# Optimization experiments

Hardware: AMD Instinct MI355X
Metric: run time of the kernel (lower is better)

The kernel has to match this reference:

```python
import jax, jax.numpy as jnp
import numpy as np

EPS = 1e-5  # torch InstanceNorm2d default eps


def instance_norm(x):
    # normalize over spatial dims (H, W) per sample, per channel; affine=False
    mean = jnp.mean(x, axis=(2, 3), keepdims=True)
    var = jnp.var(x, axis=(2, 3), keepdims=True)  # biased var, matching torch
    return (x - mean) * jax.lax.rsqrt(var + EPS)


def conv1x1(x, w, b):
    # x: [B,C,H,W], w: [O,C], b: [O] -> [B,O,H,W]
    return jnp.einsum('oc,bchw->bohw', w, x) + b[None, :, None, None]


def setup_inputs() -> dict:
    key = jax.random.key(0)
    ks = jax.random.split(key, 9)
    B, C, H, W = 4, 64, 96, 96
    fan_out = C  # 1x1 conv: fan_out = out_ch * 1 * 1
    std = float(np.sqrt(2.0 / fan_out))  # kaiming_normal_, mode='fan_out', relu
    x = jax.random.normal(ks[0], (B, C, H, W), dtype=jnp.float32)
    wq = jax.random.normal(ks[1], (C, C), dtype=jnp.float32) * std
    wk = jax.random.normal(ks[2], (C, C), dtype=jnp.float32) * std
    wv = jax.random.normal(ks[3], (C, C), dtype=jnp.float32) * std
    wo = jax.random.normal(ks[4], (C, C), dtype=jnp.float32) * std
    bq = jnp.zeros((C,), dtype=jnp.float32)
    bk = jnp.zeros((C,), dtype=jnp.float32)
    bv = jnp.zeros((C,), dtype=jnp.float32)
    bo = jnp.zeros((C,), dtype=jnp.float32)
    return {"x": x, "wq": wq, "bq": bq, "wk": wk, "bk": bk,
            "wv": wv, "bv": bv, "wo": wo, "bo": bo}


def reference(x, wq, bq, wk, bk, wv, bv, wo, bo):
    B, C, H, W = x.shape
    h = instance_norm(x)
    q = conv1x1(h, wq, bq)  # [B,C,H,W]
    k = conv1x1(h, wk, bk)
    v = conv1x1(h, wv, bv)
    N = H * W
    q = q.reshape(B, C, N).transpose(0, 2, 1)  # [B,N,C]
    k = k.reshape(B, C, N)                     # [B,C,N]
    v = v.reshape(B, C, N).transpose(0, 2, 1)  # [B,N,C]
    scores = jnp.einsum('bnc,bcm->bnm', q, k) * (C ** -0.5)  # [B,N,N]
    attn = jax.nn.softmax(scores, axis=-1)
    o = jnp.einsum('bnm,bmc->bnc', attn, v)  # [B,N,C]
    o = o.reshape(B, H, W, C).transpose(0, 3, 1, 2)  # [B,C,H,W]
    o = conv1x1(o, wo, bo)
    return x + o
```

## Files before the change

### kernel.cpp

```cpp
#include <hip/hip_runtime.h>
#include <stdint.h>

#define BB 4
#define CCH 64
#define NN 9216
#define NTILES 144
#define FTILES 72
#define NCHUNK 3
#define CHUNKK 3072

typedef unsigned short u16;
typedef __attribute__((ext_vector_type(8))) short bhalf8;
typedef __attribute__((ext_vector_type(4))) float f32x4;
typedef __attribute__((ext_vector_type(4))) u16 u16x4;
typedef __attribute__((ext_vector_type(8))) u16 u16x8;
typedef __attribute__((ext_vector_type(2))) unsigned int u32x2;

#define MFMA16(a, b, c) __builtin_amdgcn_mfma_f32_16x16x32_bf16((a), (b), (c), 0, 0, 0)

static __device__ __forceinline__ u16 f2bf(float f) {
  union { float f; unsigned u; } v; v.f = f;
  return (u16)((v.u + 0x7fffu + ((v.u >> 16) & 1u)) >> 16);
}
static __device__ __forceinline__ float bf2f(u16 h) {
  union { unsigned u; float f; } v; v.u = ((unsigned)h) << 16; return v.f;
}
static __device__ __forceinline__ unsigned pk2(float lo, float hi) {
  unsigned a = __float_as_uint(hi) + 0x8000u;
  unsigned b = __float_as_uint(lo) + 0x8000u;
  return __builtin_amdgcn_perm(a, b, 0x07060302u);
}
static __device__ __forceinline__ void glds16(const void* g, void* l) {
  __builtin_amdgcn_global_load_lds(
      (const __attribute__((address_space(1))) unsigned int*)g,
      (__attribute__((address_space(3))) unsigned int*)l, 16, 0, 0);
}

extern "C" __global__ __launch_bounds__(256) void prep_kernel(
    const float* __restrict__ x,
    const float* __restrict__ wq, const float* __restrict__ wk,
    const float* __restrict__ wv, const float* __restrict__ wo,
    float* __restrict__ mean, float* __restrict__ rstd, u16* __restrict__ wbf) {
  if (blockIdx.x >= 256) {
    int i = (blockIdx.x - 256) * 256 + threadIdx.x;
    const float* src = (i < 4096) ? wq : (i < 8192) ? wk : (i < 12288) ? wv : wo;
    wbf[i] = f2bf(src[i & 4095]);
    return;
  }
  int idx = blockIdx.x;
  const float* p = x + (size_t)idx * NN;
  float s = 0.f, ss = 0.f;
  for (int i = threadIdx.x; i < NN; i += 256) { float v = p[i]; s += v; ss += v * v; }
#pragma unroll
  for (int o = 32; o > 0; o >>= 1) { s += __shfl_xor(s, o, 64); ss += __shfl_xor(ss, o, 64); }
  __shared__ float ls[4], lss[4];
  int w = threadIdx.x >> 6;
  if ((threadIdx.x & 63) == 0) { ls[w] = s; lss[w] = ss; }
  __syncthreads();
  if (threadIdx.x == 0) {
    s = ls[0] + ls[1] + ls[2] + ls[3];
    ss = lss[0] + lss[1] + lss[2] + lss[3];
    float m = s * (1.f / NN);
    float var = ss * (1.f / NN) - m * m;
    mean[idx] = m;
    rstd[idx] = rsqrtf(var + 1e-5f);
  }
}

extern "C" __global__ __launch_bounds__(256, 4) void qkv_kernel(
    const float* __restrict__ x,
    const float* __restrict__ mean, const float* __restrict__ rstd,
    const u16* __restrict__ wqb, const u16* __restrict__ wkb, const u16* __restrict__ wvb,
    const float* __restrict__ bq, const float* __restrict__ bk,
    u16* __restrict__ Qt, u16* __restrict__ Kt, u16* __restrict__ Vt) {
  __shared__ u16 hbuf[64 * 72];
  int b = blockIdx.x / NTILES, tile = blockIdx.x % NTILES;
  int n0 = tile * 64;
  int t = threadIdx.x;
  int w = t >> 6, lane = t & 63, q = lane >> 4, ln = lane & 15;
  const float QSCALE = 0.125f * 1.44269504088896340736f;
#pragma unroll
  for (int rep = 0; rep < 16; rep++) {
    int c = rep * 4 + w;
    float v = x[(size_t)(b * 64 + c) * NN + n0 + lane];
    float h = (v - mean[b * 64 + c]) * rstd[b * 64 + c];
    hbuf[lane * 72 + c] = f2bf(h);
  }
  __syncthreads();
  int hrow = (16 * w + ln) * 72;
  bhalf8 hb0 = *(const bhalf8*)&hbuf[hrow + q * 8];
  bhalf8 hb1 = *(const bhalf8*)&hbuf[hrow + 32 + q * 8];
  size_t nrow = (size_t)(b * NN + n0 + 16 * w + ln) * 64;
#pragma unroll
  for (int ct = 0; ct < 4; ct++) {
    int wrow = (16 * ct + ln) * 64;
    bhalf8 a0 = *(const bhalf8*)&wqb[wrow + q * 8];
    bhalf8 a1 = *(const bhalf8*)&wqb[wrow + 32 + q * 8];
    f32x4 d = {0.f, 0.f, 0.f, 0.f};
    d = MFMA16(a0, hb0, d);
    d = MFMA16(a1, hb1, d);
    f32x4 b4 = *(const f32x4*)&bq[16 * ct + 4 * q];
    u16x4 pk;
#pragma unroll
    for (int r = 0; r < 4; r++) pk[r] = f2bf((d[r] + b4[r]) * QSCALE);
    *(u16x4*)&Qt[nrow + 16 * ct + 4 * q] = pk;
  }
#pragma unroll
  for (int ct = 0; ct < 4; ct++) {
    int wrow = (16 * ct + ln) * 64;
    bhalf8 a0 = *(const bhalf8*)&wkb[wrow + q * 8];
    bhalf8 a1 = *(const bhalf8*)&wkb[wrow + 32 + q * 8];
    f32x4 d = {0.f, 0.f, 0.f, 0.f};
    d = MFMA16(a0, hb0, d);
    d = MFMA16(a1, hb1, d);
    f32x4 b4 = *(const f32x4*)&bk[16 * ct + 4 * q];
    u16x4 pk;
#pragma unroll
    for (int r = 0; r < 4; r++) pk[r] = f2bf(d[r] + b4[r]);
    *(u16x4*)&Kt[nrow + 16 * ct + 4 * q] = pk;
  }
#pragma unroll
  for (int ct = 0; ct < 4; ct++) {
    int wrow = (16 * ct + ln) * 64;
    bhalf8 b0 = *(const bhalf8*)&wvb[wrow + q * 8];
    bhalf8 b1 = *(const bhalf8*)&wvb[wrow + 32 + q * 8];
    f32x4 d = {0.f, 0.f, 0.f, 0.f};
    d = MFMA16(hb0, b0, d);
    d = MFMA16(hb1, b1, d);
    u16x4 pk;
#pragma unroll
    for (int r = 0; r < 4; r++) pk[r] = f2bf(d[r]);
    *(u16x4*)&Vt[(size_t)(b * 64 + 16 * ct + ln) * NN + n0 + 16 * w + 4 * q] = pk;
  }
}

extern "C" __global__ __launch_bounds__(256, 4) void flash_kernel(
    const u16* __restrict__ Qt, const u16* __restrict__ Kt, const u16* __restrict__ Vt,
    u16* __restrict__ Opart, float* __restrict__ Lsum) {
  __shared__ u16 kbuf[64 * 64];
  __shared__ u16 vbuf[64 * 64];
  __shared__ u16 pbuf[4 * 32 * 64];
  int blk = blockIdx.x;
  int b = blk / (FTILES * NCHUNK);
  int rem = blk % (FTILES * NCHUNK);
  int tile = rem / NCHUNK, chunk = rem % NCHUNK;
  int m_start = chunk * CHUNKK;
  int t = threadIdx.x;
  int w = t >> 6, lane = t & 63, q = lane >> 4, ln = lane & 15;
  int n0w = tile * 128 + 32 * w;
  const u16* qp = Qt + (size_t)(b * NN + n0w + ln) * 64 + q * 8;
  bhalf8 qa0 = *(const bhalf8*)qp;
  bhalf8 qa1 = *(const bhalf8*)(qp + 32);
  bhalf8 qb0 = *(const bhalf8*)(qp + 16 * 64);
  bhalf8 qb1 = *(const bhalf8*)(qp + 16 * 64 + 32);
  const short ONE = 0x3F80;
  const bhalf8 ones = {ONE, ONE, ONE, ONE, ONE, ONE, ONE, ONE};
  f32x4 oa[4], ob[4];
  f32x4 lacc_a = {0.f, 0.f, 0.f, 0.f}, lacc_b = {0.f, 0.f, 0.f, 0.f};
#pragma unroll
  for (int i = 0; i < 4; i++) { oa[i] = (f32x4){0.f,0.f,0.f,0.f}; ob[i] = (f32x4){0.f,0.f,0.f,0.f}; }
  u16* pb = pbuf + w * 2048;
  int row_s = 16 * w + (lane >> 3);
  int usw = (lane & 7) ^ (row_s & 7);
  const u16* kgp = Kt + ((size_t)b * NN + m_start + row_s) * 64 + usw * 8;
  const u16* vgp = Vt + (size_t)(b * 64 + row_s) * NN + m_start + usw * 8;
  u16* klds = &kbuf[w * 1024];
  u16* vlds = &vbuf[w * 1024];
  int sbase = (q ^ (ln & 7)) * 8;

  for (int m0 = 0; m0 < CHUNKK; m0 += 64) {
    __syncthreads();
    glds16(kgp, klds);
    glds16(kgp + 512, klds + 512);
    glds16(vgp, vlds);
    glds16(vgp + (size_t)8 * NN, vlds + 512);
    kgp += 64 * 64;
    vgp += 64;
    __syncthreads();

    f32x4 sa[4], sb[4];
#pragma unroll
    for (int mt = 0; mt < 4; mt++) {
      int krow = (16 * mt + ln) * 64;
      bhalf8 ka0 = *(const bhalf8*)&kbuf[krow + sbase];
      bhalf8 ka1 = *(const bhalf8*)&kbuf[krow + (sbase ^ 32)];
      f32x4 acc = {0.f, 0.f, 0.f, 0.f};
      acc = MFMA16(ka0, qa0, acc);
      acc = MFMA16(ka1, qa1, acc);
      sa[mt] = acc;
      f32x4 acc2 = {0.f, 0.f, 0.f, 0.f};
      acc2 = MFMA16(ka0, qb0, acc2);
      acc2 = MFMA16(ka1, qb1, acc2);
      sb[mt] = acc2;
    }
#pragma unroll
    for (int mt = 0; mt < 4; mt++) {
      f32x4 pa, pbv;
#pragma unroll
      for (int r = 0; r < 4; r++) {
        pa[r] = __builtin_amdgcn_exp2f(sa[mt][r]);
        pbv[r] = __builtin_amdgcn_exp2f(sb[mt][r]);
      }
      int pu = (((2 * mt + (q >> 1)) ^ (ln & 7)) << 3) + ((q & 1) << 2);
      u32x2 pk;
      pk[0] = pk2(pa[0], pa[1]);
      pk[1] = pk2(pa[2], pa[3]);
      *(u32x2*)&pb[ln * 64 + pu] = pk;
      pk[0] = pk2(pbv[0], pbv[1]);
      pk[1] = pk2(pbv[2], pbv[3]);
      *(u32x2*)&pb[(16 + ln) * 64 + pu] = pk;
    }
#pragma unroll
    for (int s2 = 0; s2 < 2; s2++) {
      bhalf8 pfa = *(const bhalf8*)&pb[ln * 64 + (sbase ^ (32 * s2))];
      bhalf8 pfb = *(const bhalf8*)&pb[(16 + ln) * 64 + (sbase ^ (32 * s2))];
      lacc_a = MFMA16(ones, pfa, lacc_a);
      lacc_b = MFMA16(ones, pfb, lacc_b);
#pragma unroll
      for (int ct = 0; ct < 4; ct++) {
        int vrow = (16 * ct + ln) * 64;
        bhalf8 va = *(const bhalf8*)&vbuf[vrow + (sbase ^ (32 * s2))];
        oa[ct] = MFMA16(va, pfa, oa[ct]);
        ob[ct] = MFMA16(va, pfb, ob[ct]);
      }
    }
  }
  size_t pbase = (size_t)blk * (128 * 64);
  int ra = 32 * w + ln, rb = ra + 16;
#pragma unroll
  for (int ct = 0; ct < 4; ct++) {
    u32x2 pka, pkb;
    pka[0] = pk2(oa[ct][0], oa[ct][1]); pka[1] = pk2(oa[ct][2], oa[ct][3]);
    pkb[0] = pk2(ob[ct][0], ob[ct][1]); pkb[1] = pk2(ob[ct][2], ob[ct][3]);
    *(u32x2*)&Opart[pbase + (size_t)ra * 64 + 16 * ct + 4 * q] = pka;
    *(u32x2*)&Opart[pbase + (size_t)rb * 64 + 16 * ct + 4 * q] = pkb;
  }
  if (q == 0) {
    float* lb_ = Lsum + (size_t)blk * 128;
    lb_[ra] = lacc_a[0];
    lb_[rb] = lacc_b[0];
  }
}

extern "C" __global__ __launch_bounds__(256, 4) void out_kernel(
    const float* __restrict__ x, const u16* __restrict__ wob, const float* __restrict__ bo,
    const u16* __restrict__ Opart, const float* __restrict__ Lsum, const float* __restrict__ bv,
    float* __restrict__ out) {
  int b = blockIdx.x / NTILES, tile = blockIdx.x % NTILES;
  int t = threadIdx.x;
  int w = t >> 6, lane = t & 63, q = lane >> 4, ln = lane & 15;
  int n0w = tile * 64 + 16 * w;
  int ptile = tile >> 1;
  int prow = (tile & 1) * 64 + 16 * w + ln;
  int p0 = (b * FTILES + ptile) * NCHUNK;
  float L = 0.f;
  float acc0[8], acc1[8];
#pragma unroll
  for (int j = 0; j < 8; j++) { acc0[j] = 0.f; acc1[j] = 0.f; }
#pragma unroll
  for (int ch = 0; ch < NCHUNK; ch++) {
    L += Lsum[(size_t)(p0 + ch) * 128 + prow];
    const u16* op = Opart + ((size_t)(p0 + ch) * 128 + prow) * 64;
    u16x8 d0 = *(const u16x8*)(op + 8 * q);
    u16x8 d1 = *(const u16x8*)(op + 32 + 8 * q);
#pragma unroll
    for (int j = 0; j < 8; j++) { acc0[j] += bf2f(d0[j]); acc1[j] += bf2f(d1[j]); }
  }
  float rl = 1.0f / L;
  union { u16x8 us; bhalf8 bh; } A0, A1;
#pragma unroll
  for (int j = 0; j < 8; j++) {
    A0.us[j] = f2bf(acc0[j] * rl + bv[8 * q + j]);
    A1.us[j] = f2bf(acc1[j] * rl + bv[32 + 8 * q + j]);
  }
  bhalf8 a0 = A0.bh, a1 = A1.bh;
#pragma unroll
  for (int ct = 0; ct < 4; ct++) {
    int wrow = (16 * ct + ln) * 64;
    bhalf8 b0 = *(const bhalf8*)&wob[wrow + q * 8];
    bhalf8 b1 = *(const bhalf8*)&wob[wrow + 32 + q * 8];
    f32x4 d = {0.f, 0.f, 0.f, 0.f};
    d = MFMA16(a0, b0, d);
    d = MFMA16(a1, b1, d);
    int co = 16 * ct + ln;
    size_t base = (size_t)(b * 64 + co) * NN + n0w + 4 * q;
    f32x4 xv = *(const f32x4*)&x[base];
    float bc = bo[co];
    f32x4 ov;
#pragma unroll
    for (int r = 0; r < 4; r++) ov[r] = xv[r] + bc + d[r];
    *(f32x4*)&out[base] = ov;
  }
}

extern "C" void kernel_launch(void* const* d_in, const int* in_sizes, int n_in,
                              void* d_out, int out_size, void* d_ws, size_t ws_size,
                              hipStream_t stream) {
  (void)in_sizes; (void)n_in; (void)out_size; (void)ws_size;
  const float* x  = (const float*)d_in[0];
  const float* wq = (const float*)d_in[1];
  const float* bq = (const float*)d_in[2];
  const float* wk = (const float*)d_in[3];
  const float* bk = (const float*)d_in[4];
  const float* wv = (const float*)d_in[5];
  const float* bv = (const float*)d_in[6];
  const float* wo = (const float*)d_in[7];
  const float* bo = (const float*)d_in[8];
  float* out = (float*)d_out;
  char* ws = (char*)d_ws;
  float* mean = (float*)ws;
  float* rstd = (float*)(ws + 1024);
  u16* wbf = (u16*)(ws + 2048);
  u16* Qt = (u16*)(ws + 36864);
  u16* Kt = Qt + (size_t)BB * NN * 64;
  u16* Vt = Kt + (size_t)BB * NN * 64;
  u16* Opart = Vt + (size_t)BB * NN * 64;
  float* Lsum = (float*)(Opart + (size_t)BB * FTILES * NCHUNK * 128 * 64);
  const u16* wqb = wbf;
  const u16* wkb = wbf + 4096;
  const u16* wvb = wbf + 8192;
  const u16* wob = wbf + 12288;

  prep_kernel<<<320, 256, 0, stream>>>(x, wq, wk, wv, wo, mean, rstd, wbf);
  qkv_kernel<<<BB * NTILES, 256, 0, stream>>>(x, mean, rstd, wqb, wkb, wvb, bq, bk, Qt, Kt, Vt);
  flash_kernel<<<BB * FTILES * NCHUNK, 256, 0, stream>>>(Qt, Kt, Vt, Opart, Lsum);
  out_kernel<<<BB * NTILES, 256, 0, stream>>>(x, wob, bo, Opart, Lsum, bv, out);
}
```

Baseline: 220.7 us.

## Double-buffer K/V LDS tiles in flash kernel and split score/P stages into halves

The flash kernel now double-buffers the K and V shared-memory tiles, prefetching the next 64-key tile while computing on the current one. This drops one of the two barriers per iteration and hides global-to-LDS latency. The score, exp and P·V work is split into two 32-key halves with a smaller per-wave P buffer, which lowers register and LDS pressure. The qkv kernel's normalize/transpose stage also changes so each thread handles four consecutive channels and writes them to LDS as one packed store. The cost is twice the K/V LDS footprint, which may affect occupancy.

```diff
diff --git a/kernel.cpp b/kernel.cpp
--- a/kernel.cpp
+++ b/kernel.cpp
@@ -79,12 +79,20 @@
   int t = threadIdx.x;
   int w = t >> 6, lane = t & 63, q = lane >> 4, ln = lane & 15;
   const float QSCALE = 0.125f * 1.44269504088896340736f;
-#pragma unroll
-  for (int rep = 0; rep < 16; rep++) {
-    int c = rep * 4 + w;
-    float v = x[(size_t)(b * 64 + c) * NN + n0 + lane];
-    float h = (v - mean[b * 64 + c]) * rstd[b * 64 + c];
-    hbuf[lane * 72 + c] = f2bf(h);
+  const float* mb = mean + b * 64;
+  const float* rb_ = rstd + b * 64;
+  int nloc = lane;
+#pragma unroll
+  for (int rep = 0; rep < 4; rep++) {
+    int c0 = 16 * w + 4 * rep;
+    float h0 = (x[(size_t)(b * 64 + c0 + 0) * NN + n0 + nloc] - mb[c0 + 0]) * rb_[c0 + 0];
+    float h1 = (x[(size_t)(b * 64 + c0 + 1) * NN + n0 + nloc] - mb[c0 + 1]) * rb_[c0 + 1];
+    float h2 = (x[(size_t)(b * 64 + c0 + 2) * NN + n0 + nloc] - mb[c0 + 2]) * rb_[c0 + 2];
+    float h3 = (x[(size_t)(b * 64 + c0 + 3) * NN + n0 + nloc] - mb[c0 + 3]) * rb_[c0 + 3];
+    u32x2 hp;
+    hp[0] = pk2(h0, h1);
+    hp[1] = pk2(h2, h3);
+    *(u32x2*)&hbuf[nloc * 72 + c0] = hp;
   }
   __syncthreads();
   int hrow = (16 * w + ln) * 72;
@@ -137,9 +145,9 @@
 extern "C" __global__ __launch_bounds__(256, 4) void flash_kernel(
     const u16* __restrict__ Qt, const u16* __restrict__ Kt, const u16* __restrict__ Vt,
     u16* __restrict__ Opart, float* __restrict__ Lsum) {
-  __shared__ u16 kbuf[64 * 64];
-  __shared__ u16 vbuf[64 * 64];
-  __shared__ u16 pbuf[4 * 32 * 64];
+  __shared__ u16 kbuf[2][64 * 64];
+  __shared__ u16 vbuf[2][64 * 64];
+  __shared__ u16 pbuf[4][16 * 64];
   int blk = blockIdx.x;
   int b = blk / (FTILES * NCHUNK);
   int rem = blk % (FTILES * NCHUNK);
@@ -159,67 +167,76 @@
   f32x4 lacc_a = {0.f, 0.f, 0.f, 0.f}, lacc_b = {0.f, 0.f, 0.f, 0.f};
 #pragma unroll
   for (int i = 0; i < 4; i++) { oa[i] = (f32x4){0.f,0.f,0.f,0.f}; ob[i] = (f32x4){0.f,0.f,0.f,0.f}; }
-  u16* pb = pbuf + w * 2048;
+  u16* pw = pbuf[w];
   int row_s = 16 * w + (lane >> 3);
   int usw = (lane & 7) ^ (row_s & 7);
   const u16* kgp = Kt + ((size_t)b * NN + m_start + row_s) * 64 + usw * 8;
   const u16* vgp = Vt + (size_t)(b * 64 + row_s) * NN + m_start + usw * 8;
-  u16* klds = &kbuf[w * 1024];
-  u16* vlds = &vbuf[w * 1024];
   int sbase = (q ^ (ln & 7)) * 8;
-
-  for (int m0 = 0; m0 < CHUNKK; m0 += 64) {
+  const int NIT = CHUNKK / 64;
+
+  {
+    u16* kl = &kbuf[0][w * 1024];
+    u16* vl = &vbuf[0][w * 1024];
+    glds16(kgp, kl); glds16(kgp + 512, kl + 512);
+    glds16(vgp, vl); glds16(vgp + (size_t)8 * NN, vl + 512);
+    kgp += 4096; vgp += 64;
+  }
+
+#pragma unroll 2
+  for (int i = 0; i < NIT; i++) {
     __syncthreads();
-    glds16(kgp, klds);
-    glds16(kgp + 512, klds + 512);
-    glds16(vgp, vlds);
-    glds16(vgp + (size_t)8 * NN, vlds + 512);
-    kgp += 64 * 64;
-    vgp += 64;
-    __syncthreads();
-
-    f32x4 sa[4], sb[4];
-#pragma unroll
-    for (int mt = 0; mt < 4; mt++) {
-      int krow = (16 * mt + ln) * 64;
-      bhalf8 ka0 = *(const bhalf8*)&kbuf[krow + sbase];
-      bhalf8 ka1 = *(const bhalf8*)&kbuf[krow + (sbase ^ 32)];
-      f32x4 acc = {0.f, 0.f, 0.f, 0.f};
-      acc = MFMA16(ka0, qa0, acc);
-      acc = MFMA16(ka1, qa1, acc);
-      sa[mt] = acc;
-      f32x4 acc2 = {0.f, 0.f, 0.f, 0.f};
-      acc2 = MFMA16(ka0, qb0, acc2);
-      acc2 = MFMA16(ka1, qb1, acc2);
-      sb[mt] = acc2;
+    if (i + 1 < NIT) {
+      u16* kl = &kbuf[(i + 1) & 1][w * 1024];
+      u16* vl = &vbuf[(i + 1) & 1][w * 1024];
+      glds16(kgp, kl); glds16(kgp + 512, kl + 512);
+      glds16(vgp, vl); glds16(vgp + (size_t)8 * NN, vl + 512);
+      kgp += 4096; vgp += 64;
     }
-#pragma unroll
-    for (int mt = 0; mt < 4; mt++) {
-      f32x4 pa, pbv;
-#pragma unroll
-      for (int r = 0; r < 4; r++) {
-        pa[r] = __builtin_amdgcn_exp2f(sa[mt][r]);
-        pbv[r] = __builtin_amdgcn_exp2f(sb[mt][r]);
+    const u16* kb = kbuf[i & 1];
+    const u16* vb = vbuf[i & 1];
+#pragma unroll
+    for (int p = 0; p < 2; p++) {
+      f32x4 s[4];
+#pragma unroll
+      for (int lm = 0; lm < 2; lm++) {
+        int mt = 2 * p + lm;
+        int krow = (16 * mt + ln) * 64;
+        bhalf8 ka0 = *(const bhalf8*)&kb[krow + sbase];
+        bhalf8 ka1 = *(const bhalf8*)&kb[krow + (sbase ^ 32)];
+        f32x4 acc = {0.f, 0.f, 0.f, 0.f};
+        acc = MFMA16(ka0, qa0, acc);
+        acc = MFMA16(ka1, qa1, acc);
+        s[2 * lm] = acc;
+        f32x4 acc2 = {0.f, 0.f, 0.f, 0.f};
+        acc2 = MFMA16(ka0, qb0, acc2);
+        acc2 = MFMA16(ka1, qb1, acc2);
+        s[2 * lm + 1] = acc2;
       }
-      int pu = (((2 * mt + (q >> 1)) ^ (ln & 7)) << 3) + ((q & 1) << 2);
-      u32x2 pk;
-      pk[0] = pk2(pa[0], pa[1]);
-      pk[1] = pk2(pa[2], pa[3]);
-      *(u32x2*)&pb[ln * 64 + pu] = pk;
-      pk[0] = pk2(pbv[0], pbv[1]);
-      pk[1] = pk2(pbv[2], pbv[3]);
-      *(u32x2*)&pb[(16 + ln) * 64 + pu] = pk;
-    }
-#pragma unroll
-    for (int s2 = 0; s2 < 2; s2++) {
-      bhalf8 pfa = *(const bhalf8*)&pb[ln * 64 + (sbase ^ (32 * s2))];
-      bhalf8 pfb = *(const bhalf8*)&pb[(16 + ln) * 64 + (sbase ^ (32 * s2))];
+#pragma unroll
+      for (int lm = 0; lm < 2; lm++) {
+        f32x4 pa, pbv;
+#pragma unroll
+        for (int r = 0; r < 4; r++) {
+          pa[r] = __builtin_amdgcn_exp2f(s[2 * lm][r]);
+          pbv[r] = __builtin_amdgcn_exp2f(s[2 * lm + 1][r]);
+        }
+        int ua = (2 * lm + (q >> 1)) ^ (ln & 7);
+        int ub = (4 + 2 * lm + (q >> 1)) ^ (ln & 7);
+        u32x2 pka, pkb;
+        pka[0] = pk2(pa[0], pa[1]);  pka[1] = pk2(pa[2], pa[3]);
+        pkb[0] = pk2(pbv[0], pbv[1]); pkb[1] = pk2(pbv[2], pbv[3]);
+        *(u32x2*)&pw[ln * 64 + ua * 8 + (q & 1) * 4] = pka;
+        *(u32x2*)&pw[ln * 64 + ub * 8 + (q & 1) * 4] = pkb;
+      }
+      bhalf8 pfa = *(const bhalf8*)&pw[ln * 64 + ((q ^ (ln & 7)) * 8)];
+      bhalf8 pfb = *(const bhalf8*)&pw[ln * 64 + (((4 + q) ^ (ln & 7)) * 8)];
       lacc_a = MFMA16(ones, pfa, lacc_a);
       lacc_b = MFMA16(ones, pfb, lacc_b);
 #pragma unroll
       for (int ct = 0; ct < 4; ct++) {
         int vrow = (16 * ct + ln) * 64;
-        bhalf8 va = *(const bhalf8*)&vbuf[vrow + (sbase ^ (32 * s2))];
+        bhalf8 va = *(const bhalf8*)&vb[vrow + (sbase ^ (32 * p))];
         oa[ct] = MFMA16(va, pfa, oa[ct]);
         ob[ct] = MFMA16(va, pfb, ob[ct]);
       }
```

Result: no change. 220.5 us (-0.1%).
